# Optimization experiments

Hardware: AMD Instinct MI355X
Metric: run time of the kernel (lower is better)

## Reference

```python
import jax, jax.numpy as jnp
import numpy as np
import math

MODEL_DIM = 1024
DIM_K = 128
DIM_V = 128
BATCH = 8
SEQ = 2048


def setup_inputs() -> dict:
    key = jax.random.key(0)
    ks = jax.random.split(key, 6)
    return {
        "query": jax.random.normal(ks[0], (BATCH, SEQ, MODEL_DIM), dtype=jnp.float32),
        "key": jax.random.normal(ks[1], (BATCH, SEQ, MODEL_DIM), dtype=jnp.float32),
        "value": jax.random.normal(ks[2], (BATCH, SEQ, MODEL_DIM), dtype=jnp.float32),
        "Wq": jax.random.normal(ks[3], (MODEL_DIM, DIM_K), dtype=jnp.float32) * (1.0 / math.sqrt(MODEL_DIM)),
        "Wk": jax.random.normal(ks[4], (MODEL_DIM, DIM_K), dtype=jnp.float32) * (1.0 / math.sqrt(MODEL_DIM)),
        "Wv": jax.random.normal(ks[5], (MODEL_DIM, DIM_V), dtype=jnp.float32) * (1.0 / math.sqrt(MODEL_DIM)),
    }


def reference(query, key, value, Wq, Wk, Wv):
    # Projections (nn.Linear with bias=False): x @ W, W stored as [in, out]
    q = jnp.einsum("bsm,mk->bsk", query, Wq)   # [B, S, dim_k]
    k = jnp.einsum("bsm,mk->bsk", key, Wk)     # [B, S, dim_k]
    v = jnp.einsum("bsm,mv->bsv", value, Wv)   # [B, S, dim_v]

    scale = 1.0 / math.sqrt(DIM_K)
    scores = jnp.einsum("bqk,bsk->bqs", q, k) * scale  # [B, S, S]

    # is_causal=True: mask strictly-upper triangle with -inf
    seq = scores.shape[-1]
    causal = jnp.tril(jnp.ones((seq, seq), dtype=bool))  # True = keep
    scores = jnp.where(causal[None, :, :], scores, -jnp.inf)

    attn = jax.nn.softmax(scores, axis=-1)
    # NaN-fix: rows with all -inf produce NaN -> set to 0 (faithful to masked_fill of NaNs)
    attn = jnp.where(jnp.isnan(attn), 0.0, attn)

    out = jnp.einsum("bqs,bsv->bqv", attn, v)  # [B, S, dim_v]
    return out
```

## Files before the change

kernel.cpp:

```cpp
#include <hip/hip_runtime.h>
#include <hip/hip_bf16.h>
#include <math.h>

typedef short bf16x8 __attribute__((ext_vector_type(8)));
typedef float f32x4 __attribute__((ext_vector_type(4)));
typedef unsigned int u32x4 __attribute__((ext_vector_type(4)));
typedef unsigned int u32x2 __attribute__((ext_vector_type(2)));

#define SEQ 2048
#define MD 1024
#define DH 128

__device__ __forceinline__ unsigned f2b(float f) {
  union { __hip_bfloat16 h; unsigned short u; } c;
  c.h = __float2bfloat16(f);
  return (unsigned)c.u;
}

__global__ __launch_bounds__(256) void wprep_kernel(
    const float* __restrict__ wq, const float* __restrict__ wk,
    const float* __restrict__ wv, __hip_bfloat16* __restrict__ wt)
{
  const int proj = blockIdx.x;
  const int part = blockIdx.y;
  const float* __restrict__ w = (proj == 0) ? wq : ((proj == 1) ? wk : wv);
  __hip_bfloat16* __restrict__ o = wt + (size_t)proj * (128 * 1024);
  __shared__ __hip_bfloat16 t[128 * 130];
  const int tid = threadIdx.x;
#pragma unroll 4
  for (int i = 0; i < 64; ++i) {
    int idx = i * 256 + tid;
    int kl = idx >> 7, n = idx & 127;
    t[kl * 130 + n] = __float2bfloat16(w[(size_t)(part * 128 + kl) * 128 + n]);
  }
  __syncthreads();
#pragma unroll 4
  for (int j = 0; j < 64; ++j) {
    int idx = j * 256 + tid;
    int n = idx >> 7, kl = idx & 127;
    o[(size_t)n * 1024 + part * 128 + kl] = t[kl * 130 + n];
  }
}

__global__ __launch_bounds__(256) void proj_kernel(
    const float* __restrict__ xq, const float* __restrict__ xk, const float* __restrict__ xv,
    const __hip_bfloat16* __restrict__ wt,
    __hip_bfloat16* __restrict__ q_ws, __hip_bfloat16* __restrict__ k_ws,
    __hip_bfloat16* __restrict__ vt_ws)
{
  const int proj = blockIdx.y;
  const float* __restrict__ x = (proj == 0) ? xq : ((proj == 1) ? xk : xv);
  const __hip_bfloat16* __restrict__ w = wt + (size_t)proj * (128 * 1024);
  const int m0 = blockIdx.x * 64;
  const int tid = threadIdx.x;
  const int lane = tid & 63;
  const int wid = tid >> 6;
  const int ll = lane & 15, lh = lane >> 4;
  const int wr = (wid >> 1) * 32;
  const int wc = (wid & 1) * 64;

  __shared__ char lds[2][24 * 1024];

  const f32x4 zero4 = {0.f, 0.f, 0.f, 0.f};
  f32x4 acc[2][4];
#pragma unroll
  for (int mi = 0; mi < 2; ++mi)
#pragma unroll
    for (int nf = 0; nf < 4; ++nf) acc[mi][nf] = zero4;

  const int a_row = tid >> 4;
  const int a_c4  = (tid & 15) << 2;
  const int b_n   = tid >> 3;
  const int b_c   = (tid & 7) << 3;

  f32x4 ar[4];
  u32x4 br[4];

#define LD_TILES(KT)                                                          \
  {                                                                           \
    _Pragma("unroll")                                                         \
    for (int i = 0; i < 4; ++i)                                               \
      ar[i] = *reinterpret_cast<const f32x4*>(                                \
          &x[(size_t)(m0 + a_row + i * 16) * MD + (KT) * 64 + a_c4]);         \
    _Pragma("unroll")                                                         \
    for (int j = 0; j < 4; ++j)                                               \
      br[j] = *reinterpret_cast<const u32x4*>(                                \
          &w[(size_t)(b_n + j * 32) * MD + (KT) * 64 + b_c]);                 \
  }

#define ST_TILES(BUF)                                                         \
  {                                                                           \
    char* Asb = lds[BUF];                                                     \
    char* Bsb = lds[BUF] + 8192;                                              \
    _Pragma("unroll")                                                         \
    for (int i = 0; i < 4; ++i) {                                             \
      int row = a_row + i * 16;                                               \
      u32x2 pk;                                                               \
      pk[0] = f2b(ar[i][0]) | (f2b(ar[i][1]) << 16);                          \
      pk[1] = f2b(ar[i][2]) | (f2b(ar[i][3]) << 16);                          \
      *reinterpret_cast<u32x2*>(Asb + row * 128 +                             \
          ((a_c4 << 1) ^ ((row & 7) << 4))) = pk;                             \
    }                                                                         \
    _Pragma("unroll")                                                         \
    for (int j = 0; j < 4; ++j) {                                             \
      int n = b_n + j * 32;                                                   \
      *reinterpret_cast<u32x4*>(Bsb + n * 128 +                               \
          ((b_c << 1) ^ ((n & 7) << 4))) = br[j];                             \
    }                                                                         \
  }

  const int kt0 = ((blockIdx.x * 7) + (blockIdx.y * 5)) & 15;

  LD_TILES(kt0);
  ST_TILES(0);
  __syncthreads();

  for (int t = 0; t < 16; ++t) {
    const int cur = t & 1;
    if (t < 15) LD_TILES((kt0 + t + 1) & 15);
    {
      char* Asb = lds[cur];
      char* Bsb = lds[cur] + 8192;
#pragma unroll
      for (int kk = 0; kk < 2; ++kk) {
        bf16x8 af[2], bfv[4];
#pragma unroll
        for (int mi = 0; mi < 2; ++mi) {
          int row = wr + mi * 16 + ll;
          af[mi] = *reinterpret_cast<bf16x8*>(
              Asb + row * 128 + ((kk * 64 + lh * 16) ^ ((row & 7) << 4)));
        }
#pragma unroll
        for (int nf = 0; nf < 4; ++nf) {
          int n = wc + nf * 16 + ll;
          bfv[nf] = *reinterpret_cast<bf16x8*>(
              Bsb + n * 128 + ((kk * 64 + lh * 16) ^ ((n & 7) << 4)));
        }
#pragma unroll
        for (int mi = 0; mi < 2; ++mi)
#pragma unroll
          for (int nf = 0; nf < 4; ++nf)
            acc[mi][nf] = __builtin_amdgcn_mfma_f32_16x16x32_bf16(
                af[mi], bfv[nf], acc[mi][nf], 0, 0, 0);
      }
    }
    if (t < 15) ST_TILES(1 - cur);
    __syncthreads();
  }
#undef LD_TILES
#undef ST_TILES

  if (proj < 2) {
    __hip_bfloat16* __restrict__ outp = proj ? k_ws : q_ws;
#pragma unroll
    for (int mi = 0; mi < 2; ++mi)
#pragma unroll
      for (int nf = 0; nf < 4; ++nf) {
        int col = wc + nf * 16 + ll;
#pragma unroll
        for (int q = 0; q < 4; ++q) {
          int row = m0 + wr + mi * 16 + lh * 4 + q;
          union { __hip_bfloat16 h; unsigned short u; } c;
          c.u = (unsigned short)f2b(acc[mi][nf][q]);
          outp[(size_t)row * DH + col] = c.h;
        }
      }
  } else {
    const int b = m0 >> 11, sb = m0 & 2047;
#pragma unroll
    for (int mi = 0; mi < 2; ++mi)
#pragma unroll
      for (int nf = 0; nf < 4; ++nf) {
        int s = sb + wr + mi * 16 + lh * 4;
        int d = wc + nf * 16 + ll;
        u32x2 pk;
        pk[0] = f2b(acc[mi][nf][0]) | (f2b(acc[mi][nf][1]) << 16);
        pk[1] = f2b(acc[mi][nf][2]) | (f2b(acc[mi][nf][3]) << 16);
        *reinterpret_cast<u32x2*>(&vt_ws[((size_t)b * DH + d) * SEQ + s]) = pk;
      }
  }
}

__global__ __launch_bounds__(256) void attn_kernel(
    const __hip_bfloat16* __restrict__ q_ws, const __hip_bfloat16* __restrict__ k_ws,
    const __hip_bfloat16* __restrict__ vt_ws,
    float* __restrict__ pO, float* __restrict__ pml)
{
  const int s = blockIdx.x;
  int qt, c;
  if (s < 8)       { qt = s;                c = 0; }
  else if (s < 24) { int u = s - 8;  qt = 8 + (u >> 1);  c = u & 1; }
  else if (s < 48) { int u = s - 24; qt = 16 + u / 3;    c = u % 3; }
  else             { int u = s - 48; qt = 24 + (u >> 2); c = u & 3; }
  const int b = blockIdx.y;
  const int g = qt >> 3;
  const int slot = b * 80 + (4 * g * (g + 1) + (g + 1) * (qt & 7)) + c;

  const int tid = threadIdx.x;
  const int lane = tid & 63;
  const int wid = tid >> 6;
  const int ll = lane & 15;
  const int lh = lane >> 4;

  __shared__ __hip_bfloat16 Ks[64 * 128];
  __shared__ __hip_bfloat16 Vs[128 * 64];
  __shared__ float Ps[64 * 64];
  char* Ksb = (char*)Ks;
  char* Vsb = (char*)Vs;
  char* Psb = (char*)Ps;

  bf16x8 qf[4];
  {
    const size_t qbase = ((size_t)b * SEQ + qt * 64 + wid * 16 + ll) * DH;
#pragma unroll
    for (int kk = 0; kk < 4; ++kk)
      qf[kk] = *reinterpret_cast<const bf16x8*>(&q_ws[qbase + kk * 32 + lh * 8]);
  }

  const f32x4 zero4 = {0.f, 0.f, 0.f, 0.f};
  float m_r[4], l_r[4];
  f32x4 oacc[8];
#pragma unroll
  for (int q = 0; q < 4; ++q) { m_r[q] = -INFINITY; l_r[q] = 0.f; }
#pragma unroll
  for (int nd = 0; nd < 8; ++nd) oacc[nd] = zero4;

  const float sl2e = 0.0883883476483184f * 1.4426950408889634f;

  const int it0 = c * 8;
  const int it1 = min(qt + 1, it0 + 8);
  for (int it = it0; it < it1; ++it) {
    const int kv0 = it * 64;
#pragma unroll
    for (int i = 0; i < 4; ++i) {
      int id = tid + i * 256;
      int row = id >> 4;
      int cb = (id & 15) << 4;
      u32x4 v = *reinterpret_cast<const u32x4*>(
          &k_ws[((size_t)b * SEQ + kv0 + row) * DH + (cb >> 1)]);
      *reinterpret_cast<u32x4*>(Ksb + row * 256 + (cb ^ ((row & 7) << 4))) = v;
    }
#pragma unroll
    for (int i = 0; i < 4; ++i) {
      int id = tid + i * 256;
      int d = id >> 3;
      int cb = (id & 7) << 4;
      u32x4 v = *reinterpret_cast<const u32x4*>(
          &vt_ws[((size_t)b * DH + d) * SEQ + kv0 + (cb >> 1)]);
      *reinterpret_cast<u32x4*>(Vsb + d * 128 + (cb ^ ((d & 7) << 4))) = v;
    }
    __syncthreads();

    f32x4 sacc[4];
#pragma unroll
    for (int nf = 0; nf < 4; ++nf) sacc[nf] = zero4;
#pragma unroll
    for (int nf = 0; nf < 4; ++nf) {
      int row = nf * 16 + ll;
#pragma unroll
      for (int kk = 0; kk < 4; ++kk) {
        bf16x8 kf = *reinterpret_cast<bf16x8*>(
            Ksb + row * 256 + ((kk * 64 + lh * 16) ^ ((row & 7) << 4)));
        sacc[nf] = __builtin_amdgcn_mfma_f32_16x16x32_bf16(qf[kk], kf, sacc[nf], 0, 0, 0);
      }
    }

    float sv[4][4];
    const int qr0 = qt * 64 + wid * 16 + lh * 4;
#pragma unroll
    for (int nf = 0; nf < 4; ++nf) {
      int kc = kv0 + nf * 16 + ll;
#pragma unroll
      for (int q = 0; q < 4; ++q) {
        float sc = sacc[nf][q] * sl2e;
        sv[nf][q] = (kc <= qr0 + q) ? sc : -INFINITY;
      }
    }

    float p[4][4];
    float alpha[4];
#pragma unroll
    for (int q = 0; q < 4; ++q) {
      float mx = fmaxf(fmaxf(sv[0][q], sv[1][q]), fmaxf(sv[2][q], sv[3][q]));
#pragma unroll
      for (int off = 1; off < 16; off <<= 1)
        mx = fmaxf(mx, __shfl_xor(mx, off));
      float mnew = fmaxf(m_r[q], mx);
      float sum = 0.f;
#pragma unroll
      for (int nf = 0; nf < 4; ++nf) {
        float pv = exp2f(sv[nf][q] - mnew);
        p[nf][q] = pv;
        sum += pv;
      }
#pragma unroll
      for (int off = 1; off < 16; off <<= 1)
        sum += __shfl_xor(sum, off);
      alpha[q] = exp2f(m_r[q] - mnew);
      l_r[q] = l_r[q] * alpha[q] + sum;
      m_r[q] = mnew;
    }
#pragma unroll
    for (int nd = 0; nd < 8; ++nd)
#pragma unroll
      for (int q = 0; q < 4; ++q) oacc[nd][q] *= alpha[q];

#pragma unroll
    for (int nf = 0; nf < 4; ++nf) {
      int kv = nf * 16 + ll;
      f32x4 pv4 = {p[nf][0], p[nf][1], p[nf][2], p[nf][3]};
      *reinterpret_cast<f32x4*>(
          Psb + kv * 256 + ((wid * 64 + lh * 16) ^ ((kv & 7) << 4))) = pv4;
    }

#pragma unroll
    for (int kf = 0; kf < 2; ++kf) {
      float pf[8];
#pragma unroll
      for (int j = 0; j < 8; ++j) {
        int kv = kf * 32 + lh * 8 + j;
        pf[j] = *reinterpret_cast<float*>(
            Psb + kv * 256 + ((wid * 64 + ll * 4) ^ ((kv & 7) << 4)));
      }
      bf16x8 pa;
#pragma unroll
      for (int j = 0; j < 8; ++j) pa[j] = (short)f2b(pf[j]);
#pragma unroll
      for (int nd = 0; nd < 8; ++nd) {
        int d = nd * 16 + ll;
        bf16x8 vf = *reinterpret_cast<bf16x8*>(
            Vsb + d * 128 + ((kf * 64 + lh * 16) ^ ((d & 7) << 4)));
        oacc[nd] = __builtin_amdgcn_mfma_f32_16x16x32_bf16(pa, vf, oacc[nd], 0, 0, 0);
      }
    }
    __syncthreads();
  }

  float* __restrict__ po = pO + (size_t)slot * (64 * 128);
#pragma unroll
  for (int nd = 0; nd < 8; ++nd) {
    int d = nd * 16 + ll;
#pragma unroll
    for (int q = 0; q < 4; ++q) {
      int row = wid * 16 + lh * 4 + q;
      po[row * 128 + d] = oacc[nd][q];
    }
  }
  if (ll == 0) {
    float* __restrict__ pm = pml + (size_t)slot * 128;
#pragma unroll
    for (int q = 0; q < 4; ++q) {
      int row = wid * 16 + lh * 4 + q;
      pm[row * 2 + 0] = m_r[q];
      pm[row * 2 + 1] = l_r[q];
    }
  }
}

__global__ __launch_bounds__(256) void combine_kernel(
    const float* __restrict__ pO, const float* __restrict__ pml,
    float* __restrict__ out)
{
  const int qt = blockIdx.x;
  const int b = blockIdx.y;
  const int g = qt >> 3;
  const int nc = g + 1;
  const size_t slot0 = (size_t)b * 80 + (4 * g * (g + 1) + (g + 1) * (qt & 7));
  const int tid = threadIdx.x;
  const int r = tid >> 2;
  const int q4 = tid & 3;

  float m[4], l[4];
#pragma unroll
  for (int i = 0; i < 4; ++i) {
    if (i < nc) {
      m[i] = pml[(slot0 + i) * 128 + r * 2 + 0];
      l[i] = pml[(slot0 + i) * 128 + r * 2 + 1];
    } else { m[i] = -INFINITY; l[i] = 0.f; }
  }
  float M = fmaxf(fmaxf(m[0], m[1]), fmaxf(m[2], m[3]));
  float w[4];
  float L = 0.f;
#pragma unroll
  for (int i = 0; i < 4; ++i) {
    w[i] = (i < nc) ? exp2f(m[i] - M) : 0.f;
    L += l[i] * w[i];
  }
  const float inv = 1.0f / L;

  const size_t orow = ((size_t)b * SEQ + qt * 64 + r) * DH;
#pragma unroll
  for (int j = 0; j < 8; ++j) {
    const int col = q4 * 32 + j * 4;
    f32x4 acc = {0.f, 0.f, 0.f, 0.f};
#pragma unroll
    for (int i = 0; i < 4; ++i) {
      if (i < nc) {
        f32x4 v = *reinterpret_cast<const f32x4*>(
            &pO[(slot0 + i) * (64 * 128) + r * 128 + col]);
#pragma unroll
        for (int u = 0; u < 4; ++u) acc[u] += v[u] * w[i];
      }
    }
#pragma unroll
    for (int u = 0; u < 4; ++u) acc[u] *= inv;
    *reinterpret_cast<f32x4*>(&out[orow + col]) = acc;
  }
}

extern "C" void kernel_launch(void* const* d_in, const int* in_sizes, int n_in,
                              void* d_out, int out_size, void* d_ws, size_t ws_size,
                              hipStream_t stream) {
  const float* xq = (const float*)d_in[0];
  const float* xk = (const float*)d_in[1];
  const float* xv = (const float*)d_in[2];
  const float* wq = (const float*)d_in[3];
  const float* wk = (const float*)d_in[4];
  const float* wv = (const float*)d_in[5];

  __hip_bfloat16* q_ws = (__hip_bfloat16*)d_ws;
  __hip_bfloat16* k_ws = q_ws + (size_t)16384 * 128;
  __hip_bfloat16* vt_ws = k_ws + (size_t)16384 * 128;
  __hip_bfloat16* wt_ws = vt_ws + (size_t)16384 * 128;
  float* pO = (float*)((char*)d_ws + 13369344);
  float* pml = (float*)((char*)d_ws + 13369344 + 20971520);
  float* out = (float*)d_out;

  wprep_kernel<<<dim3(3, 8), 256, 0, stream>>>(wq, wk, wv, wt_ws);
  proj_kernel<<<dim3(256, 3), 256, 0, stream>>>(xq, xk, xv, wt_ws,
                                                q_ws, k_ws, vt_ws);
  attn_kernel<<<dim3(80, 8), 256, 0, stream>>>(q_ws, k_ws, vt_ws, pO, pml);
  combine_kernel<<<dim3(32, 8), 256, 0, stream>>>(pO, pml, out);
}
```

Before: 103.5 us.

## Deepen projection GEMM global-load prefetch to three register stages

The projection kernel now keeps three K-tiles of global loads in flight in registers instead of one, fully unrolls the 16-step K loop, and writes the next tile into the other LDS buffer before the MFMA work rather than after it. It also drops the per-block staggered starting K offset and sets a launch-bounds occupancy hint of 3. The aim is to hide more global memory latency in this bandwidth-heavy fp32-input GEMM. The cost is more registers, and the LDS stores now sit ahead of the compute, which may stall on load latency. Removing the stagger may also raise channel contention.

```diff
diff --git a/kernel.cpp b/kernel.cpp
--- a/kernel.cpp
+++ b/kernel.cpp
@@ -42,7 +42,7 @@
   }
 }
 
-__global__ __launch_bounds__(256) void proj_kernel(
+__global__ __launch_bounds__(256, 3) void proj_kernel(
     const float* __restrict__ xq, const float* __restrict__ xk, const float* __restrict__ xv,
     const __hip_bfloat16* __restrict__ wt,
     __hip_bfloat16* __restrict__ q_ws, __hip_bfloat16* __restrict__ k_ws,
@@ -73,22 +73,25 @@
   const int b_n   = tid >> 3;
   const int b_c   = (tid & 7) << 3;
 
-  f32x4 ar[4];
-  u32x4 br[4];
-
-#define LD_TILES(KT)                                                          \
+  const float* __restrict__ xbase = x + (size_t)(m0 + a_row) * MD + a_c4;
+  const __hip_bfloat16* __restrict__ wbase = w + (size_t)b_n * MD + b_c;
+
+  f32x4 ar[3][4];
+  u32x4 br[3][4];
+
+#define LD_TILES(KT, S)                                                       \
   {                                                                           \
     _Pragma("unroll")                                                         \
     for (int i = 0; i < 4; ++i)                                               \
-      ar[i] = *reinterpret_cast<const f32x4*>(                                \
-          &x[(size_t)(m0 + a_row + i * 16) * MD + (KT) * 64 + a_c4]);         \
+      ar[S][i] = *reinterpret_cast<const f32x4*>(                             \
+          xbase + (size_t)i * 16 * MD + (KT) * 64);                           \
     _Pragma("unroll")                                                         \
     for (int j = 0; j < 4; ++j)                                               \
-      br[j] = *reinterpret_cast<const u32x4*>(                                \
-          &w[(size_t)(b_n + j * 32) * MD + (KT) * 64 + b_c]);                 \
-  }
-
-#define ST_TILES(BUF)                                                         \
+      br[S][j] = *reinterpret_cast<const u32x4*>(                             \
+          wbase + (size_t)j * 32 * MD + (KT) * 64);                           \
+  }
+
+#define ST_TILES(S, BUF)                                                      \
   {                                                                           \
     char* Asb = lds[BUF];                                                     \
     char* Bsb = lds[BUF] + 8192;                                              \
@@ -96,8 +99,8 @@
     for (int i = 0; i < 4; ++i) {                                             \
       int row = a_row + i * 16;                                               \
       u32x2 pk;                                                               \
-      pk[0] = f2b(ar[i][0]) | (f2b(ar[i][1]) << 16);                          \
-      pk[1] = f2b(ar[i][2]) | (f2b(ar[i][3]) << 16);                          \
+      pk[0] = f2b(ar[S][i][0]) | (f2b(ar[S][i][1]) << 16);                    \
+      pk[1] = f2b(ar[S][i][2]) | (f2b(ar[S][i][3]) << 16);                    \
       *reinterpret_cast<u32x2*>(Asb + row * 128 +                             \
           ((a_c4 << 1) ^ ((row & 7) << 4))) = pk;                             \
     }                                                                         \
@@ -105,19 +108,21 @@
     for (int j = 0; j < 4; ++j) {                                             \
       int n = b_n + j * 32;                                                   \
       *reinterpret_cast<u32x4*>(Bsb + n * 128 +                               \
-          ((b_c << 1) ^ ((n & 7) << 4))) = br[j];                             \
+          ((b_c << 1) ^ ((n & 7) << 4))) = br[S][j];                          \
     }                                                                         \
   }
 
-  const int kt0 = ((blockIdx.x * 7) + (blockIdx.y * 5)) & 15;
-
-  LD_TILES(kt0);
-  ST_TILES(0);
+  LD_TILES(0, 0);
+  LD_TILES(1, 1);
+  LD_TILES(2, 2);
+  ST_TILES(0, 0);
   __syncthreads();
 
+#pragma unroll
   for (int t = 0; t < 16; ++t) {
     const int cur = t & 1;
-    if (t < 15) LD_TILES((kt0 + t + 1) & 15);
+    if (t + 3 < 16) LD_TILES(t + 3, (t + 3) % 3);
+    if (t + 1 < 16) ST_TILES((t + 1) % 3, cur ^ 1);
     {
       char* Asb = lds[cur];
       char* Bsb = lds[cur] + 8192;
@@ -144,7 +149,6 @@
                 af[mi], bfv[nf], acc[mi][nf], 0, 0, 0);
       }
     }
-    if (t < 15) ST_TILES(1 - cur);
     __syncthreads();
   }
 #undef LD_TILES
```

After: 103.2 us. No clear change (-0.3%).

## Store partial attention outputs in bf16 and remove staggered k-tile start

Applied to the files above, without the earlier changes.

The attention kernel now writes its split-K partial outputs in bf16 instead of fp32, which halves the intermediate buffer. The combine kernel reads them as 8-wide bf16 vectors and widens them to fp32 before the weighted reduction. This cuts write and read traffic for the partial results, at the cost of rounding the unnormalized partial outputs to bf16. The projection kernel also drops its per-block staggered starting k-tile and iterates the tiles from zero, which may change cache and channel contention when many blocks load the same columns.

```diff
diff --git a/kernel.cpp b/kernel.cpp
--- a/kernel.cpp
+++ b/kernel.cpp
@@ -109,15 +109,13 @@
     }                                                                         \
   }
 
-  const int kt0 = ((blockIdx.x * 7) + (blockIdx.y * 5)) & 15;
-
-  LD_TILES(kt0);
+  LD_TILES(0);
   ST_TILES(0);
   __syncthreads();
 
-  for (int t = 0; t < 16; ++t) {
-    const int cur = t & 1;
-    if (t < 15) LD_TILES((kt0 + t + 1) & 15);
+  for (int kt = 0; kt < 16; ++kt) {
+    const int cur = kt & 1;
+    if (kt < 15) LD_TILES(kt + 1);
     {
       char* Asb = lds[cur];
       char* Bsb = lds[cur] + 8192;
@@ -144,7 +142,7 @@
                 af[mi], bfv[nf], acc[mi][nf], 0, 0, 0);
       }
     }
-    if (t < 15) ST_TILES(1 - cur);
+    if (kt < 15) ST_TILES(1 - cur);
     __syncthreads();
   }
 #undef LD_TILES
@@ -184,7 +182,7 @@
 __global__ __launch_bounds__(256) void attn_kernel(
     const __hip_bfloat16* __restrict__ q_ws, const __hip_bfloat16* __restrict__ k_ws,
     const __hip_bfloat16* __restrict__ vt_ws,
-    float* __restrict__ pO, float* __restrict__ pml)
+    __hip_bfloat16* __restrict__ pO, float* __restrict__ pml)
 {
   const int s = blockIdx.x;
   int qt, c;
@@ -336,14 +334,16 @@
     __syncthreads();
   }
 
-  float* __restrict__ po = pO + (size_t)slot * (64 * 128);
+  __hip_bfloat16* __restrict__ po = pO + (size_t)slot * (64 * 128);
 #pragma unroll
   for (int nd = 0; nd < 8; ++nd) {
     int d = nd * 16 + ll;
 #pragma unroll
     for (int q = 0; q < 4; ++q) {
       int row = wid * 16 + lh * 4 + q;
-      po[row * 128 + d] = oacc[nd][q];
+      union { __hip_bfloat16 h; unsigned short u; } cc;
+      cc.u = (unsigned short)f2b(oacc[nd][q]);
+      po[row * 128 + d] = cc.h;
     }
   }
   if (ll == 0) {
@@ -358,7 +358,7 @@
 }
 
 __global__ __launch_bounds__(256) void combine_kernel(
-    const float* __restrict__ pO, const float* __restrict__ pml,
+    const __hip_bfloat16* __restrict__ pO, const float* __restrict__ pml,
     float* __restrict__ out)
 {
   const int qt = blockIdx.x;
@@ -390,21 +390,29 @@
 
   const size_t orow = ((size_t)b * SEQ + qt * 64 + r) * DH;
 #pragma unroll
-  for (int j = 0; j < 8; ++j) {
-    const int col = q4 * 32 + j * 4;
-    f32x4 acc = {0.f, 0.f, 0.f, 0.f};
+  for (int j = 0; j < 4; ++j) {
+    const int col = q4 * 32 + j * 8;
+    float acc[8];
+#pragma unroll
+    for (int u = 0; u < 8; ++u) acc[u] = 0.f;
 #pragma unroll
     for (int i = 0; i < 4; ++i) {
       if (i < nc) {
-        f32x4 v = *reinterpret_cast<const f32x4*>(
+        bf16x8 v = *reinterpret_cast<const bf16x8*>(
             &pO[(slot0 + i) * (64 * 128) + r * 128 + col]);
 #pragma unroll
-        for (int u = 0; u < 4; ++u) acc[u] += v[u] * w[i];
-      }
-    }
-#pragma unroll
-    for (int u = 0; u < 4; ++u) acc[u] *= inv;
-    *reinterpret_cast<f32x4*>(&out[orow + col]) = acc;
+        for (int u = 0; u < 8; ++u) {
+          union { unsigned u32; float f; } cv;
+          cv.u32 = ((unsigned)(unsigned short)v[u]) << 16;
+          acc[u] += cv.f * w[i];
+        }
+      }
+    }
+    f32x4 o0, o1;
+#pragma unroll
+    for (int u = 0; u < 4; ++u) { o0[u] = acc[u] * inv; o1[u] = acc[4 + u] * inv; }
+    *reinterpret_cast<f32x4*>(&out[orow + col]) = o0;
+    *reinterpret_cast<f32x4*>(&out[orow + col + 4]) = o1;
   }
 }
 
@@ -422,8 +430,8 @@
   __hip_bfloat16* k_ws = q_ws + (size_t)16384 * 128;
   __hip_bfloat16* vt_ws = k_ws + (size_t)16384 * 128;
   __hip_bfloat16* wt_ws = vt_ws + (size_t)16384 * 128;
-  float* pO = (float*)((char*)d_ws + 13369344);
-  float* pml = (float*)((char*)d_ws + 13369344 + 20971520);
+  __hip_bfloat16* pO = (__hip_bfloat16*)((char*)d_ws + 13369344);
+  float* pml = (float*)((char*)d_ws + 13369344 + 10485760);
   float* out = (float*)d_out;
 
   wprep_kernel<<<dim3(3, 8), 256, 0, stream>>>(wq, wk, wv, wt_ws);
```

After: 96.16 us, median of 2. -7.1%, faster.
